# Performance work log

Measured on AMD Instinct MI355X. Metric: run time of the kernel, lower is better.

## Reference

```python
import jax, jax.numpy as jnp
import numpy as np

N_NODES = 50000
N_EDGES = 800000
D_IN = 128
D_OUT = 128
NEG_SLOPE = 0.2


def setup_inputs() -> dict:
    key = jax.random.key(0)
    ks = jax.random.split(key, 6)
    stdv = 1.0 / np.sqrt(D_OUT)
    X = jax.random.normal(ks[0], (N_NODES, D_IN), dtype=jnp.float32)
    W = jax.random.uniform(ks[1], (D_IN, D_OUT), dtype=jnp.float32, minval=-stdv, maxval=stdv)
    W_r = jax.random.uniform(ks[2], (D_IN, D_OUT), dtype=jnp.float32, minval=-stdv, maxval=stdv)
    W_l = jax.random.uniform(ks[3], (D_IN, D_OUT), dtype=jnp.float32, minval=-stdv, maxval=stdv)
    src = jax.random.randint(ks[4], (N_EDGES,), 0, N_NODES, dtype=jnp.int32)
    dst = jax.random.randint(ks[5], (N_EDGES,), 0, N_NODES, dtype=jnp.int32)
    return {"X": X, "W": W, "W_r": W_r, "W_l": W_l, "src": src, "dst": dst}


def reference(X, W, W_r, W_l, src, dst):
    # Dense transforms (comb/agg feature paths)
    comb = X @ W            # [N, D_out]
    h_r = X @ W_r           # [N, D_out]
    h_l = X @ W_l           # [N, D_out]
    # SDDMM: per-edge score e_ij = dot(h_l[i], h_r[j]) at nonzeros of A
    e = jnp.sum(h_l[src] * h_r[dst], axis=-1)          # [E]
    e = jax.nn.leaky_relu(e, negative_slope=NEG_SLOPE)  # LeakyReLU(0.2) on edge values
    # SpMM aggregation: agg[i] = sum_{j in N(i)} e_ij * comb[j]
    msgs = e[:, None] * comb[dst]                       # [E, D_out]
    agg = jax.ops.segment_sum(msgs, src, num_segments=N_NODES)  # [N, D_out]
    return agg
```

## Files before the change

kernel.cpp:

```cpp
#include <hip/hip_runtime.h>
#include <hip/hip_bf16.h>

#define N_NODES 50000
#define N_EDGES 800000
#define D 128
#define NEG_SLOPE 0.2f
#define APAD 136

#define FB 196
#define BCAP 8192
#define CHUNK 4096
#define BIN_NBLK ((N_EDGES + CHUNK - 1) / CHUNK)
#define GROWS 64
#define GGRID ((N_NODES + GROWS - 1) / GROWS)

typedef __attribute__((ext_vector_type(8))) short bf16x8;
typedef __attribute__((ext_vector_type(4))) float f32x4;

__device__ inline unsigned short f2bf(float f) {
    union { float f; unsigned u; } v; v.f = f;
    const unsigned r = v.u + 0x7FFF + ((v.u >> 16) & 1);
    return (unsigned short)(r >> 16);
}
__device__ inline unsigned fbits(float f) { union { float f; unsigned u; } v; v.f = f; return v.u; }
__device__ inline float ffrom(unsigned u) { union { unsigned u; float f; } v; v.u = u; return v.f; }

__device__ inline void unpack8(const float4 raw, float* o) {
    const unsigned w0 = fbits(raw.x), w1 = fbits(raw.y), w2 = fbits(raw.z), w3 = fbits(raw.w);
    o[0] = ffrom(w0 << 16); o[1] = ffrom(w0 & 0xffff0000u);
    o[2] = ffrom(w1 << 16); o[3] = ffrom(w1 & 0xffff0000u);
    o[4] = ffrom(w2 << 16); o[5] = ffrom(w2 & 0xffff0000u);
    o[6] = ffrom(w3 << 16); o[7] = ffrom(w3 & 0xffff0000u);
}

__device__ inline int scan256_incl(int* arr, int t, int v) {
    arr[t] = v; __syncthreads();
#pragma unroll
    for (int off = 1; off < 256; off <<= 1) {
        const int u = (t >= off) ? arr[t - off] : 0;
        __syncthreads();
        arr[t] += u;
        __syncthreads();
    }
    return arr[t];
}

__device__ __forceinline__ void stage_B_lds(unsigned short* Bs, const ushort* __restrict__ BT) {
    const int tid = threadIdx.x;
#pragma unroll
    for (int i = 0; i < 8; ++i) {
        const int idx = tid + i * 256;
        const int row = idx >> 4;
        const int c8 = (idx & 15) << 3;
        const float4 v = ((const float4*)BT)[idx];
        *(float4*)&Bs[row * APAD + c8] = v;
    }
}

template <bool OUT_F32>
__device__ __forceinline__ void mfma_from_lds(const unsigned short* Bs,
                                              const unsigned short* As,
                                              int rb, float* __restrict__ Cf,
                                              ushort* __restrict__ Cb, int nrows) {
    const int tid = threadIdx.x;
    const int w = tid >> 6, lane = tid & 63, m = lane & 15, kq = lane >> 4;
    f32x4 acc[8] = {};
    const unsigned short* Arow = &As[(w * 16 + m) * APAD + kq * 8];
#pragma unroll
    for (int kc = 0; kc < 4; ++kc) {
        const bf16x8 af = *(const bf16x8*)(Arow + kc * 32);
#pragma unroll
        for (int t2 = 0; t2 < 8; ++t2) {
            const bf16x8 bf = *(const bf16x8*)&Bs[(t2 * 16 + m) * APAD + kc * 32 + kq * 8];
            acc[t2] = __builtin_amdgcn_mfma_f32_16x16x32_bf16(af, bf, acc[t2], 0, 0, 0);
        }
    }
    const int orow0 = rb + w * 16 + kq * 4;
#pragma unroll
    for (int t2 = 0; t2 < 8; ++t2) {
#pragma unroll
        for (int r = 0; r < 4; ++r) {
            const int row = orow0 + r;
            if (row < nrows) {
                const size_t o = (size_t)row * D + t2 * 16 + m;
                if (OUT_F32) Cf[o] = acc[t2][r];
                else         Cb[o] = f2bf(acc[t2][r]);
            }
        }
    }
}

__global__ __launch_bounds__(256) void bin_prep_kernel(const int* __restrict__ src,
                                                       const int* __restrict__ dst,
                                                       int* __restrict__ bucket_fill,
                                                       int2* __restrict__ binned,
                                                       const float* __restrict__ W_l,
                                                       const float* __restrict__ W_r,
                                                       const float* __restrict__ W,
                                                       ushort* __restrict__ MbT,
                                                       ushort* __restrict__ WbT) {
    if (blockIdx.x < BIN_NBLK) {
        __shared__ int hist[256];
        __shared__ int bstart[256];
        __shared__ int reserveS[256];
        __shared__ int fillL[256];
        __shared__ int2 pairs[CHUNK];
        __shared__ int targ[CHUNK];
        const int t = threadIdx.x;
        const int e0 = blockIdx.x * CHUNK;

        hist[t] = 0;
        __syncthreads();

        int s[16], d[16], b[16];
#pragma unroll
        for (int i = 0; i < 16; ++i) {
            const int e = e0 + i * 256 + t;
            if (e < N_EDGES) {
                s[i] = src[e]; d[i] = dst[e]; b[i] = s[i] >> 8;
                atomicAdd(&hist[b[i]], 1);
            } else b[i] = -1;
        }
        __syncthreads();
        const int hv = hist[t];
        const int incl = scan256_incl(bstart, t, hv);
        const int mystart = incl - hv;
        reserveS[t] = hv ? atomicAdd(&bucket_fill[t], hv) : 0;
        __syncthreads();
        bstart[t] = mystart;
        fillL[t] = mystart;
        __syncthreads();
#pragma unroll
        for (int i = 0; i < 16; ++i) {
            if (b[i] >= 0) {
                const int p = atomicAdd(&fillL[b[i]], 1);
                pairs[p] = make_int2(s[i], d[i]);
                const int pos = reserveS[b[i]] + (p - bstart[b[i]]);
                targ[p] = (pos < BCAP) ? (b[i] * BCAP + pos) : -1;
            }
        }
        __syncthreads();
        const int nval = min(CHUNK, N_EDGES - e0);
        for (int j = t; j < nval; j += 256)
            if (targ[j] >= 0) binned[targ[j]] = pairs[j];
    } else {
        const int a = (blockIdx.x - BIN_NBLK) * 2 + (threadIdx.x >> 7);
        const int b2 = threadIdx.x & 127;
        float acc = 0.f;
#pragma unroll
        for (int c = 0; c < D; c += 4) {
            const float4 wl = *(const float4*)(W_l + a * D + c);
            const float4 wr = *(const float4*)(W_r + b2 * D + c);
            acc += wl.x * wr.x + wl.y * wr.y + wl.z * wr.z + wl.w * wr.w;
        }
        MbT[b2 * D + a] = f2bf(acc);
        WbT[b2 * D + a] = f2bf(W[a * D + b2]);
    }
}

__global__ __launch_bounds__(256) void convert_gemm1_kernel(const float4* __restrict__ Xf4,
                                                            ushort* __restrict__ Xb,
                                                            const ushort* __restrict__ MbT,
                                                            ushort* __restrict__ hMb) {
    __shared__ __align__(16) unsigned short Bs[D * APAD];
    __shared__ __align__(16) unsigned short As[GROWS * APAD];
    const int t = threadIdx.x;
    const int rb = blockIdx.x * GROWS;

    stage_B_lds(Bs, MbT);

#pragma unroll
    for (int i = 0; i < 4; ++i) {
        const int f2 = t + i * 256;
        const int row = f2 >> 4;
        const int c8 = (f2 & 15) << 3;
        ushort4 lo = {0, 0, 0, 0}, hi = {0, 0, 0, 0};
        if (rb + row < N_NODES) {
            const float4 a = Xf4[(size_t)(rb + row) * 32 + (c8 >> 2)];
            const float4 b = Xf4[(size_t)(rb + row) * 32 + (c8 >> 2) + 1];
            lo.x = f2bf(a.x); lo.y = f2bf(a.y); lo.z = f2bf(a.z); lo.w = f2bf(a.w);
            hi.x = f2bf(b.x); hi.y = f2bf(b.y); hi.z = f2bf(b.z); hi.w = f2bf(b.w);
            ushort* gp = Xb + (size_t)(rb + row) * D + c8;
            *(ushort4*)gp = lo;
            *(ushort4*)(gp + 4) = hi;
        }
        *(ushort4*)&As[row * APAD + c8] = lo;
        *(ushort4*)&As[row * APAD + c8 + 4] = hi;
    }
    __syncthreads();
    mfma_from_lds<false>(Bs, As, rb, nullptr, hMb, N_NODES);
}

__global__ __launch_bounds__(256) void fine_kernel(const int2* __restrict__ binned,
                                                   const int* __restrict__ bucket_fill,
                                                   int* __restrict__ offsets,
                                                   int* __restrict__ sorted_dst) {
    __shared__ int cntS[256];
    __shared__ int nh[256];
    __shared__ int ex[256];
    __shared__ int fill[256];
    __shared__ int dstbuf[BCAP];
    const int b = blockIdx.x;
    const int t = threadIdx.x;

    const int myc = (t < FB) ? bucket_fill[t] : 0;
    scan256_incl(cntS, t, myc);
    const int base = (b == 0) ? 0 : cntS[b - 1];
    int cnt = cntS[b] - base;
    if (cnt > BCAP) cnt = BCAP;

    nh[t] = 0;
    __syncthreads();
    const int2* bb = binned + (size_t)b * BCAP;
    for (int e = t; e < cnt; e += 256) atomicAdd(&nh[bb[e].x & 255], 1);
    __syncthreads();
    const int v = nh[t];
    const int incl2 = scan256_incl(ex, t, v);
    const int mystart = incl2 - v;
    const int node = b * 256 + t;
    if (node < N_NODES) offsets[node] = base + mystart;
    fill[t] = mystart;
    __syncthreads();
    for (int e = t; e < cnt; e += 256) {
        const int2 sd = bb[e];
        const int p = atomicAdd(&fill[sd.x & 255], 1);
        dstbuf[p] = sd.y;
    }
    __syncthreads();
    for (int j = t; j < cnt; j += 256)
        sorted_dst[base + j] = dstbuf[j];
}

__global__ __launch_bounds__(256) void spmm_gemm2_kernel(const ushort* __restrict__ hMb,
                                                         const ushort* __restrict__ Xb,
                                                         const int* __restrict__ offsets,
                                                         const int* __restrict__ sorted_dst,
                                                         const ushort* __restrict__ WbT,
                                                         float* __restrict__ agg) {
    __shared__ __align__(16) unsigned short Bs[D * APAD];
    __shared__ __align__(16) unsigned short aggl[GROWS * APAD];
    const int t = threadIdx.x;
    const int rb = blockIdx.x * GROWS;
    const int lane = t & 63, w = t >> 6;
    const int q = lane >> 4, ql = lane & 15;
    const int qid = w * 4 + q;

    stage_B_lds(Bs, WbT);

    for (int i = 0; i < 4; ++i) {
        const int node = rb + qid * 4 + i;
        float acc[8] = {0.f, 0.f, 0.f, 0.f, 0.f, 0.f, 0.f, 0.f};
        if (node < N_NODES) {
            float hm[8];
            unpack8(*(const float4*)(hMb + (size_t)node * D + ql * 8), hm);
            const int start = offsets[node];
            const int end = (node == N_NODES - 1) ? N_EDGES : offsets[node + 1];
            int idx = start;
            while (idx + 3 < end) {
                const int d0 = sorted_dst[idx];
                const int d1 = sorted_dst[idx + 1];
                const int d2 = sorted_dst[idx + 2];
                const int d3 = sorted_dst[idx + 3];
                const float4 r0 = *(const float4*)(Xb + (size_t)d0 * D + ql * 8);
                const float4 r1 = *(const float4*)(Xb + (size_t)d1 * D + ql * 8);
                const float4 r2 = *(const float4*)(Xb + (size_t)d2 * D + ql * 8);
                const float4 r3 = *(const float4*)(Xb + (size_t)d3 * D + ql * 8);
                float t0 = 0.f, t1 = 0.f, t2 = 0.f, t3 = 0.f;
                {
                    float x[8];
                    unpack8(r0, x);
#pragma unroll
                    for (int j = 0; j < 8; ++j) t0 = fmaf(hm[j], x[j], t0);
                    unpack8(r1, x);
#pragma unroll
                    for (int j = 0; j < 8; ++j) t1 = fmaf(hm[j], x[j], t1);
                    unpack8(r2, x);
#pragma unroll
                    for (int j = 0; j < 8; ++j) t2 = fmaf(hm[j], x[j], t2);
                    unpack8(r3, x);
#pragma unroll
                    for (int j = 0; j < 8; ++j) t3 = fmaf(hm[j], x[j], t3);
                }
#pragma unroll
                for (int mm = 1; mm < 16; mm <<= 1) {
                    t0 += __shfl_xor(t0, mm);
                    t1 += __shfl_xor(t1, mm);
                    t2 += __shfl_xor(t2, mm);
                    t3 += __shfl_xor(t3, mm);
                }
                const float e0 = t0 > 0.f ? t0 : NEG_SLOPE * t0;
                const float e1 = t1 > 0.f ? t1 : NEG_SLOPE * t1;
                const float e2 = t2 > 0.f ? t2 : NEG_SLOPE * t2;
                const float e3 = t3 > 0.f ? t3 : NEG_SLOPE * t3;
                {
                    float x[8];
                    unpack8(r0, x);
#pragma unroll
                    for (int j = 0; j < 8; ++j) acc[j] = fmaf(e0, x[j], acc[j]);
                    unpack8(r1, x);
#pragma unroll
                    for (int j = 0; j < 8; ++j) acc[j] = fmaf(e1, x[j], acc[j]);
                    unpack8(r2, x);
#pragma unroll
                    for (int j = 0; j < 8; ++j) acc[j] = fmaf(e2, x[j], acc[j]);
                    unpack8(r3, x);
#pragma unroll
                    for (int j = 0; j < 8; ++j) acc[j] = fmaf(e3, x[j], acc[j]);
                }
                idx += 4;
            }
            while (idx < end) {
                const int d0 = sorted_dst[idx];
                const float4 r0 = *(const float4*)(Xb + (size_t)d0 * D + ql * 8);
                float x[8];
                unpack8(r0, x);
                float t0 = 0.f;
#pragma unroll
                for (int j = 0; j < 8; ++j) t0 = fmaf(hm[j], x[j], t0);
#pragma unroll
                for (int mm = 1; mm < 16; mm <<= 1) t0 += __shfl_xor(t0, mm);
                const float e0 = t0 > 0.f ? t0 : NEG_SLOPE * t0;
#pragma unroll
                for (int j = 0; j < 8; ++j) acc[j] = fmaf(e0, x[j], acc[j]);
                ++idx;
            }
        }
        ushort4 o0, o1;
        o0.x = f2bf(acc[0]); o0.y = f2bf(acc[1]); o0.z = f2bf(acc[2]); o0.w = f2bf(acc[3]);
        o1.x = f2bf(acc[4]); o1.y = f2bf(acc[5]); o1.z = f2bf(acc[6]); o1.w = f2bf(acc[7]);
        unsigned short* lp = &aggl[(qid * 4 + i) * APAD + ql * 8];
        *(ushort4*)lp = o0;
        *(ushort4*)(lp + 4) = o1;
    }
    __syncthreads();
    mfma_from_lds<true>(Bs, aggl, rb, agg, nullptr, N_NODES);
}

extern "C" void kernel_launch(void* const* d_in, const int* in_sizes, int n_in,
                              void* d_out, int out_size, void* d_ws, size_t ws_size,
                              hipStream_t stream) {
    const float* X   = (const float*)d_in[0];
    const float* W   = (const float*)d_in[1];
    const float* W_r = (const float*)d_in[2];
    const float* W_l = (const float*)d_in[3];
    const int* src   = (const int*)d_in[4];
    const int* dst   = (const int*)d_in[5];
    float* agg = (float*)d_out;

    ushort* Xb          = (ushort*)d_ws;
    ushort* hMb         = Xb + (size_t)N_NODES * D;
    ushort* MbT         = hMb + (size_t)N_NODES * D;
    ushort* WbT         = MbT + D * D;
    int*    offsets     = (int*)(WbT + D * D);
    int*    sorted_dst  = offsets + N_NODES;
    int*    bucket_fill = sorted_dst + N_EDGES;
    int2*   binned      = (int2*)(bucket_fill + 256);

    hipMemsetAsync(bucket_fill, 0, 256 * sizeof(int), stream);

    bin_prep_kernel<<<BIN_NBLK + 64, 256, 0, stream>>>(
        src, dst, bucket_fill, binned, W_l, W_r, W, MbT, WbT);

    fine_kernel<<<FB, 256, 0, stream>>>(binned, bucket_fill, offsets, sorted_dst);

    convert_gemm1_kernel<<<GGRID, 256, 0, stream>>>(
        (const float4*)X, Xb, MbT, hMb);

    spmm_gemm2_kernel<<<GGRID, 256, 0, stream>>>(
        hMb, Xb, offsets, sorted_dst, WbT, agg);
}
```

Measured before the change: 185.7 us.

## Restructure pipeline: fuse binning with GEMM1, split SpMM per-wave from GEMM2

Weight precomputation moves into a small prep kernel that also zeroes bucket counters, which removes the memset. Edge binning now runs in the same launch as the X conversion and first GEMM, using a shared LDS union and smaller chunks. The SpMM becomes one wave per node with four edge lanes, reduced by shuffles, and writes bf16 aggregates to a buffer that a separate GEMM2 kernel consumes. The fine sort uses 512 threads. This trades an extra global round trip of the aggregates and one more launch for better load balance and parallelism in the gather.

Measured after the change: 169.6 us. 8.7% less time.

```diff
diff --git a/kernel.cpp b/kernel.cpp
--- a/kernel.cpp
+++ b/kernel.cpp
@@ -9,10 +9,11 @@
 
 #define FB 196
 #define BCAP 8192
-#define CHUNK 4096
+#define CHUNK 2048
 #define BIN_NBLK ((N_EDGES + CHUNK - 1) / CHUNK)
 #define GROWS 64
 #define GGRID ((N_NODES + GROWS - 1) / GROWS)
+#define GEMM_LDS (D * APAD * 2 + GROWS * APAD * 2)
 
 typedef __attribute__((ext_vector_type(8))) short bf16x8;
 typedef __attribute__((ext_vector_type(4))) float f32x4;
@@ -90,31 +91,53 @@
     }
 }
 
-__global__ __launch_bounds__(256) void bin_prep_kernel(const int* __restrict__ src,
-                                                       const int* __restrict__ dst,
-                                                       int* __restrict__ bucket_fill,
-                                                       int2* __restrict__ binned,
-                                                       const float* __restrict__ W_l,
-                                                       const float* __restrict__ W_r,
-                                                       const float* __restrict__ W,
-                                                       ushort* __restrict__ MbT,
-                                                       ushort* __restrict__ WbT) {
-    if (blockIdx.x < BIN_NBLK) {
-        __shared__ int hist[256];
-        __shared__ int bstart[256];
-        __shared__ int reserveS[256];
-        __shared__ int fillL[256];
-        __shared__ int2 pairs[CHUNK];
-        __shared__ int targ[CHUNK];
-        const int t = threadIdx.x;
-        const int e0 = blockIdx.x * CHUNK;
+__global__ __launch_bounds__(256) void prep_kernel(const float* __restrict__ W_l,
+                                                   const float* __restrict__ W_r,
+                                                   const float* __restrict__ W,
+                                                   ushort* __restrict__ MbT,
+                                                   ushort* __restrict__ WbT,
+                                                   int* __restrict__ bucket_fill) {
+    if (blockIdx.x == 0) bucket_fill[threadIdx.x] = 0;
+    const int a = blockIdx.x * 2 + (threadIdx.x >> 7);
+    const int b2 = threadIdx.x & 127;
+    float acc = 0.f;
+#pragma unroll
+    for (int c = 0; c < D; c += 4) {
+        const float4 wl = *(const float4*)(W_l + a * D + c);
+        const float4 wr = *(const float4*)(W_r + b2 * D + c);
+        acc += wl.x * wr.x + wl.y * wr.y + wl.z * wr.z + wl.w * wr.w;
+    }
+    MbT[b2 * D + a] = f2bf(acc);
+    WbT[b2 * D + a] = f2bf(W[a * D + b2]);
+}
+
+__global__ __launch_bounds__(256) void k1_kernel(const int* __restrict__ src,
+                                                 const int* __restrict__ dst,
+                                                 int* __restrict__ bucket_fill,
+                                                 int2* __restrict__ binned,
+                                                 const ushort* __restrict__ MbT,
+                                                 const float4* __restrict__ Xf4,
+                                                 ushort* __restrict__ Xb,
+                                                 ushort* __restrict__ hMb) {
+    __shared__ __align__(16) char smem[GEMM_LDS];
+    const int bx = blockIdx.x;
+    const int t = threadIdx.x;
+
+    if (bx < BIN_NBLK) {
+        int*  hist     = (int*)smem;
+        int*  bstart   = hist + 256;
+        int*  reserveS = bstart + 256;
+        int*  fillL    = reserveS + 256;
+        int2* pairs    = (int2*)(fillL + 256);
+        int*  targ     = (int*)(pairs + CHUNK);
+        const int e0 = bx * CHUNK;
 
         hist[t] = 0;
         __syncthreads();
 
-        int s[16], d[16], b[16];
-#pragma unroll
-        for (int i = 0; i < 16; ++i) {
+        int s[8], d[8], b[8];
+#pragma unroll
+        for (int i = 0; i < 8; ++i) {
             const int e = e0 + i * 256 + t;
             if (e < N_EDGES) {
                 s[i] = src[e]; d[i] = dst[e]; b[i] = s[i] >> 8;
@@ -131,7 +154,7 @@
         fillL[t] = mystart;
         __syncthreads();
 #pragma unroll
-        for (int i = 0; i < 16; ++i) {
+        for (int i = 0; i < 8; ++i) {
             if (b[i] >= 0) {
                 const int p = atomicAdd(&fillL[b[i]], 1);
                 pairs[p] = make_int2(s[i], d[i]);
@@ -144,54 +167,35 @@
         for (int j = t; j < nval; j += 256)
             if (targ[j] >= 0) binned[targ[j]] = pairs[j];
     } else {
-        const int a = (blockIdx.x - BIN_NBLK) * 2 + (threadIdx.x >> 7);
-        const int b2 = threadIdx.x & 127;
-        float acc = 0.f;
-#pragma unroll
-        for (int c = 0; c < D; c += 4) {
-            const float4 wl = *(const float4*)(W_l + a * D + c);
-            const float4 wr = *(const float4*)(W_r + b2 * D + c);
-            acc += wl.x * wr.x + wl.y * wr.y + wl.z * wr.z + wl.w * wr.w;
-        }
-        MbT[b2 * D + a] = f2bf(acc);
-        WbT[b2 * D + a] = f2bf(W[a * D + b2]);
-    }
-}
-
-__global__ __launch_bounds__(256) void convert_gemm1_kernel(const float4* __restrict__ Xf4,
-                                                            ushort* __restrict__ Xb,
-                                                            const ushort* __restrict__ MbT,
-                                                            ushort* __restrict__ hMb) {
-    __shared__ __align__(16) unsigned short Bs[D * APAD];
-    __shared__ __align__(16) unsigned short As[GROWS * APAD];
-    const int t = threadIdx.x;
-    const int rb = blockIdx.x * GROWS;
-
-    stage_B_lds(Bs, MbT);
-
-#pragma unroll
-    for (int i = 0; i < 4; ++i) {
-        const int f2 = t + i * 256;
-        const int row = f2 >> 4;
-        const int c8 = (f2 & 15) << 3;
-        ushort4 lo = {0, 0, 0, 0}, hi = {0, 0, 0, 0};
-        if (rb + row < N_NODES) {
-            const float4 a = Xf4[(size_t)(rb + row) * 32 + (c8 >> 2)];
-            const float4 b = Xf4[(size_t)(rb + row) * 32 + (c8 >> 2) + 1];
-            lo.x = f2bf(a.x); lo.y = f2bf(a.y); lo.z = f2bf(a.z); lo.w = f2bf(a.w);
-            hi.x = f2bf(b.x); hi.y = f2bf(b.y); hi.z = f2bf(b.z); hi.w = f2bf(b.w);
-            ushort* gp = Xb + (size_t)(rb + row) * D + c8;
-            *(ushort4*)gp = lo;
-            *(ushort4*)(gp + 4) = hi;
-        }
-        *(ushort4*)&As[row * APAD + c8] = lo;
-        *(ushort4*)&As[row * APAD + c8 + 4] = hi;
-    }
-    __syncthreads();
-    mfma_from_lds<false>(Bs, As, rb, nullptr, hMb, N_NODES);
-}
-
-__global__ __launch_bounds__(256) void fine_kernel(const int2* __restrict__ binned,
+        unsigned short* Bs = (unsigned short*)smem;
+        unsigned short* As = Bs + D * APAD;
+        const int rb = (bx - BIN_NBLK) * GROWS;
+
+        stage_B_lds(Bs, MbT);
+#pragma unroll
+        for (int i = 0; i < 4; ++i) {
+            const int f2 = t + i * 256;
+            const int row = f2 >> 4;
+            const int c8 = (f2 & 15) << 3;
+            ushort4 lo = {0, 0, 0, 0}, hi = {0, 0, 0, 0};
+            if (rb + row < N_NODES) {
+                const float4 a = Xf4[(size_t)(rb + row) * 32 + (c8 >> 2)];
+                const float4 b = Xf4[(size_t)(rb + row) * 32 + (c8 >> 2) + 1];
+                lo.x = f2bf(a.x); lo.y = f2bf(a.y); lo.z = f2bf(a.z); lo.w = f2bf(a.w);
+                hi.x = f2bf(b.x); hi.y = f2bf(b.y); hi.z = f2bf(b.z); hi.w = f2bf(b.w);
+                ushort* gp = Xb + (size_t)(rb + row) * D + c8;
+                *(ushort4*)gp = lo;
+                *(ushort4*)(gp + 4) = hi;
+            }
+            *(ushort4*)&As[row * APAD + c8] = lo;
+            *(ushort4*)&As[row * APAD + c8 + 4] = hi;
+        }
+        __syncthreads();
+        mfma_from_lds<false>(Bs, As, rb, nullptr, hMb, N_NODES);
+    }
+}
+
+__global__ __launch_bounds__(512) void fine_kernel(const int2* __restrict__ binned,
                                                    const int* __restrict__ bucket_fill,
                                                    int* __restrict__ offsets,
                                                    int* __restrict__ sorted_dst) {
@@ -203,137 +207,177 @@
     const int b = blockIdx.x;
     const int t = threadIdx.x;
 
-    const int myc = (t < FB) ? bucket_fill[t] : 0;
-    scan256_incl(cntS, t, myc);
+    if (t < 256) cntS[t] = (t < FB) ? bucket_fill[t] : 0;
+    __syncthreads();
+#pragma unroll
+    for (int off = 1; off < 256; off <<= 1) {
+        const int u = (t >= off && t < 256) ? cntS[t - off] : 0;
+        __syncthreads();
+        if (t < 256) cntS[t] += u;
+        __syncthreads();
+    }
     const int base = (b == 0) ? 0 : cntS[b - 1];
     int cnt = cntS[b] - base;
     if (cnt > BCAP) cnt = BCAP;
 
-    nh[t] = 0;
+    if (t < 256) nh[t] = 0;
     __syncthreads();
     const int2* bb = binned + (size_t)b * BCAP;
-    for (int e = t; e < cnt; e += 256) atomicAdd(&nh[bb[e].x & 255], 1);
-    __syncthreads();
-    const int v = nh[t];
-    const int incl2 = scan256_incl(ex, t, v);
-    const int mystart = incl2 - v;
-    const int node = b * 256 + t;
-    if (node < N_NODES) offsets[node] = base + mystart;
-    fill[t] = mystart;
-    __syncthreads();
-    for (int e = t; e < cnt; e += 256) {
+    for (int e = t; e < cnt; e += 512) atomicAdd(&nh[bb[e].x & 255], 1);
+    __syncthreads();
+    const int v = (t < 256) ? nh[t] : 0;
+    if (t < 256) ex[t] = v;
+    __syncthreads();
+#pragma unroll
+    for (int off = 1; off < 256; off <<= 1) {
+        const int u = (t >= off && t < 256) ? ex[t - off] : 0;
+        __syncthreads();
+        if (t < 256) ex[t] += u;
+        __syncthreads();
+    }
+    if (t < 256) {
+        const int mystart = ex[t] - v;
+        const int node = b * 256 + t;
+        if (node < N_NODES) offsets[node] = base + mystart;
+        fill[t] = mystart;
+    }
+    __syncthreads();
+    for (int e = t; e < cnt; e += 512) {
         const int2 sd = bb[e];
         const int p = atomicAdd(&fill[sd.x & 255], 1);
         dstbuf[p] = sd.y;
     }
     __syncthreads();
-    for (int j = t; j < cnt; j += 256)
+    for (int j = t; j < cnt; j += 512)
         sorted_dst[base + j] = dstbuf[j];
 }
 
-__global__ __launch_bounds__(256) void spmm_gemm2_kernel(const ushort* __restrict__ hMb,
-                                                         const ushort* __restrict__ Xb,
-                                                         const int* __restrict__ offsets,
-                                                         const int* __restrict__ sorted_dst,
-                                                         const ushort* __restrict__ WbT,
-                                                         float* __restrict__ agg) {
-    __shared__ __align__(16) unsigned short Bs[D * APAD];
-    __shared__ __align__(16) unsigned short aggl[GROWS * APAD];
-    const int t = threadIdx.x;
-    const int rb = blockIdx.x * GROWS;
-    const int lane = t & 63, w = t >> 6;
-    const int q = lane >> 4, ql = lane & 15;
-    const int qid = w * 4 + q;
-
-    stage_B_lds(Bs, WbT);
-
-    for (int i = 0; i < 4; ++i) {
-        const int node = rb + qid * 4 + i;
-        float acc[8] = {0.f, 0.f, 0.f, 0.f, 0.f, 0.f, 0.f, 0.f};
-        if (node < N_NODES) {
-            float hm[8];
-            unpack8(*(const float4*)(hMb + (size_t)node * D + ql * 8), hm);
-            const int start = offsets[node];
-            const int end = (node == N_NODES - 1) ? N_EDGES : offsets[node + 1];
-            int idx = start;
-            while (idx + 3 < end) {
-                const int d0 = sorted_dst[idx];
-                const int d1 = sorted_dst[idx + 1];
-                const int d2 = sorted_dst[idx + 2];
-                const int d3 = sorted_dst[idx + 3];
-                const float4 r0 = *(const float4*)(Xb + (size_t)d0 * D + ql * 8);
-                const float4 r1 = *(const float4*)(Xb + (size_t)d1 * D + ql * 8);
-                const float4 r2 = *(const float4*)(Xb + (size_t)d2 * D + ql * 8);
-                const float4 r3 = *(const float4*)(Xb + (size_t)d3 * D + ql * 8);
-                float t0 = 0.f, t1 = 0.f, t2 = 0.f, t3 = 0.f;
-                {
-                    float x[8];
-                    unpack8(r0, x);
-#pragma unroll
-                    for (int j = 0; j < 8; ++j) t0 = fmaf(hm[j], x[j], t0);
-                    unpack8(r1, x);
-#pragma unroll
-                    for (int j = 0; j < 8; ++j) t1 = fmaf(hm[j], x[j], t1);
-                    unpack8(r2, x);
-#pragma unroll
-                    for (int j = 0; j < 8; ++j) t2 = fmaf(hm[j], x[j], t2);
-                    unpack8(r3, x);
-#pragma unroll
-                    for (int j = 0; j < 8; ++j) t3 = fmaf(hm[j], x[j], t3);
-                }
-#pragma unroll
-                for (int mm = 1; mm < 16; mm <<= 1) {
-                    t0 += __shfl_xor(t0, mm);
-                    t1 += __shfl_xor(t1, mm);
-                    t2 += __shfl_xor(t2, mm);
-                    t3 += __shfl_xor(t3, mm);
-                }
-                const float e0 = t0 > 0.f ? t0 : NEG_SLOPE * t0;
-                const float e1 = t1 > 0.f ? t1 : NEG_SLOPE * t1;
-                const float e2 = t2 > 0.f ? t2 : NEG_SLOPE * t2;
-                const float e3 = t3 > 0.f ? t3 : NEG_SLOPE * t3;
-                {
-                    float x[8];
-                    unpack8(r0, x);
-#pragma unroll
-                    for (int j = 0; j < 8; ++j) acc[j] = fmaf(e0, x[j], acc[j]);
-                    unpack8(r1, x);
-#pragma unroll
-                    for (int j = 0; j < 8; ++j) acc[j] = fmaf(e1, x[j], acc[j]);
-                    unpack8(r2, x);
-#pragma unroll
-                    for (int j = 0; j < 8; ++j) acc[j] = fmaf(e2, x[j], acc[j]);
-                    unpack8(r3, x);
-#pragma unroll
-                    for (int j = 0; j < 8; ++j) acc[j] = fmaf(e3, x[j], acc[j]);
-                }
-                idx += 4;
-            }
-            while (idx < end) {
-                const int d0 = sorted_dst[idx];
-                const float4 r0 = *(const float4*)(Xb + (size_t)d0 * D + ql * 8);
-                float x[8];
-                unpack8(r0, x);
-                float t0 = 0.f;
-#pragma unroll
-                for (int j = 0; j < 8; ++j) t0 = fmaf(hm[j], x[j], t0);
-#pragma unroll
-                for (int mm = 1; mm < 16; mm <<= 1) t0 += __shfl_xor(t0, mm);
-                const float e0 = t0 > 0.f ? t0 : NEG_SLOPE * t0;
-#pragma unroll
-                for (int j = 0; j < 8; ++j) acc[j] = fmaf(e0, x[j], acc[j]);
-                ++idx;
-            }
-        }
+__global__ __launch_bounds__(256) void spmm_kernel(const ushort* __restrict__ hMb,
+                                                   const ushort* __restrict__ Xb,
+                                                   const int* __restrict__ offsets,
+                                                   const int* __restrict__ sorted_dst,
+                                                   ushort* __restrict__ aggXb) {
+    const int wave = threadIdx.x >> 6;
+    const int lane = threadIdx.x & 63;
+    const int node = blockIdx.x * 4 + wave;
+    const int q = lane >> 4;
+    const int ql = lane & 15;
+
+    float hm[8];
+    unpack8(*(const float4*)(hMb + (size_t)node * D + ql * 8), hm);
+
+    const int start = offsets[node];
+    const int end = (node == N_NODES - 1) ? N_EDGES : offsets[node + 1];
+
+    float acc[8] = {0.f, 0.f, 0.f, 0.f, 0.f, 0.f, 0.f, 0.f};
+
+    int idx = start + q;
+    while (idx + 12 < end) {
+        const int d0 = sorted_dst[idx];
+        const int d1 = sorted_dst[idx + 4];
+        const int d2 = sorted_dst[idx + 8];
+        const int d3 = sorted_dst[idx + 12];
+        const float4 r0 = *(const float4*)(Xb + (size_t)d0 * D + ql * 8);
+        const float4 r1 = *(const float4*)(Xb + (size_t)d1 * D + ql * 8);
+        const float4 r2 = *(const float4*)(Xb + (size_t)d2 * D + ql * 8);
+        const float4 r3 = *(const float4*)(Xb + (size_t)d3 * D + ql * 8);
+        float t0 = 0.f, t1 = 0.f, t2 = 0.f, t3 = 0.f;
+        {
+            float x[8];
+            unpack8(r0, x);
+#pragma unroll
+            for (int j = 0; j < 8; ++j) t0 = fmaf(hm[j], x[j], t0);
+            unpack8(r1, x);
+#pragma unroll
+            for (int j = 0; j < 8; ++j) t1 = fmaf(hm[j], x[j], t1);
+            unpack8(r2, x);
+#pragma unroll
+            for (int j = 0; j < 8; ++j) t2 = fmaf(hm[j], x[j], t2);
+            unpack8(r3, x);
+#pragma unroll
+            for (int j = 0; j < 8; ++j) t3 = fmaf(hm[j], x[j], t3);
+        }
+#pragma unroll
+        for (int mm = 1; mm < 16; mm <<= 1) {
+            t0 += __shfl_xor(t0, mm);
+            t1 += __shfl_xor(t1, mm);
+            t2 += __shfl_xor(t2, mm);
+            t3 += __shfl_xor(t3, mm);
+        }
+        const float e0 = t0 > 0.f ? t0 : NEG_SLOPE * t0;
+        const float e1 = t1 > 0.f ? t1 : NEG_SLOPE * t1;
+        const float e2 = t2 > 0.f ? t2 : NEG_SLOPE * t2;
+        const float e3 = t3 > 0.f ? t3 : NEG_SLOPE * t3;
+        {
+            float x[8];
+            unpack8(r0, x);
+#pragma unroll
+            for (int j = 0; j < 8; ++j) acc[j] = fmaf(e0, x[j], acc[j]);
+            unpack8(r1, x);
+#pragma unroll
+            for (int j = 0; j < 8; ++j) acc[j] = fmaf(e1, x[j], acc[j]);
+            unpack8(r2, x);
+#pragma unroll
+            for (int j = 0; j < 8; ++j) acc[j] = fmaf(e2, x[j], acc[j]);
+            unpack8(r3, x);
+#pragma unroll
+            for (int j = 0; j < 8; ++j) acc[j] = fmaf(e3, x[j], acc[j]);
+        }
+        idx += 16;
+    }
+    while (idx < end) {
+        const int d0 = sorted_dst[idx];
+        const float4 r0 = *(const float4*)(Xb + (size_t)d0 * D + ql * 8);
+        float x[8];
+        unpack8(r0, x);
+        float t0 = 0.f;
+#pragma unroll
+        for (int j = 0; j < 8; ++j) t0 = fmaf(hm[j], x[j], t0);
+#pragma unroll
+        for (int mm = 1; mm < 16; mm <<= 1) t0 += __shfl_xor(t0, mm);
+        const float e0 = t0 > 0.f ? t0 : NEG_SLOPE * t0;
+#pragma unroll
+        for (int j = 0; j < 8; ++j) acc[j] = fmaf(e0, x[j], acc[j]);
+        idx += 4;
+    }
+
+#pragma unroll
+    for (int j = 0; j < 8; ++j) {
+        acc[j] += __shfl_xor(acc[j], 16);
+        acc[j] += __shfl_xor(acc[j], 32);
+    }
+    if (q == 0) {
         ushort4 o0, o1;
         o0.x = f2bf(acc[0]); o0.y = f2bf(acc[1]); o0.z = f2bf(acc[2]); o0.w = f2bf(acc[3]);
         o1.x = f2bf(acc[4]); o1.y = f2bf(acc[5]); o1.z = f2bf(acc[6]); o1.w = f2bf(acc[7]);
-        unsigned short* lp = &aggl[(qid * 4 + i) * APAD + ql * 8];
-        *(ushort4*)lp = o0;
-        *(ushort4*)(lp + 4) = o1;
-    }
-    __syncthreads();
-    mfma_from_lds<true>(Bs, aggl, rb, agg, nullptr, N_NODES);
+        ushort* outp = aggXb + (size_t)node * D + ql * 8;
+        *(ushort4*)outp = o0;
+        *(ushort4*)(outp + 4) = o1;
+    }
+}
+
+__global__ __launch_bounds__(256) void gemm2_kernel(const ushort* __restrict__ A,
+                                                    const ushort* __restrict__ BT,
+                                                    float* __restrict__ Cf) {
+    __shared__ __align__(16) char smem[GEMM_LDS];
+    unsigned short* Bs = (unsigned short*)smem;
+    unsigned short* As = Bs + D * APAD;
+    const int tid = threadIdx.x;
+    const int rb = blockIdx.x * GROWS;
+
+    stage_B_lds(Bs, BT);
+#pragma unroll
+    for (int i = 0; i < 4; ++i) {
+        const int idx = tid + i * 256;
+        const int row = idx >> 4;
+        const int c8 = (idx & 15) << 3;
+        float4 v = {0.f, 0.f, 0.f, 0.f};
+        if (rb + row < N_NODES)
+            v = ((const float4*)(A + (size_t)(rb + row) * D))[idx & 15];
+        *(float4*)&As[row * APAD + c8] = v;
+    }
+    __syncthreads();
+    mfma_from_lds<true>(Bs, As, rb, Cf, nullptr, N_NODES);
 }
 
 extern "C" void kernel_launch(void* const* d_in, const int* in_sizes, int n_in,
@@ -349,23 +393,22 @@
 
     ushort* Xb          = (ushort*)d_ws;
     ushort* hMb         = Xb + (size_t)N_NODES * D;
-    ushort* MbT         = hMb + (size_t)N_NODES * D;
+    ushort* aggXb       = hMb + (size_t)N_NODES * D;
+    ushort* MbT         = aggXb + (size_t)N_NODES * D;
     ushort* WbT         = MbT + D * D;
     int*    offsets     = (int*)(WbT + D * D);
     int*    sorted_dst  = offsets + N_NODES;
     int*    bucket_fill = sorted_dst + N_EDGES;
     int2*   binned      = (int2*)(bucket_fill + 256);
 
-    hipMemsetAsync(bucket_fill, 0, 256 * sizeof(int), stream);
-
-    bin_prep_kernel<<<BIN_NBLK + 64, 256, 0, stream>>>(
-        src, dst, bucket_fill, binned, W_l, W_r, W, MbT, WbT);
-
-    fine_kernel<<<FB, 256, 0, stream>>>(binned, bucket_fill, offsets, sorted_dst);
-
-    convert_gemm1_kernel<<<GGRID, 256, 0, stream>>>(
-        (const float4*)X, Xb, MbT, hMb);
-
-    spmm_gemm2_kernel<<<GGRID, 256, 0, stream>>>(
-        hMb, Xb, offsets, sorted_dst, WbT, agg);
-}
+    prep_kernel<<<64, 256, 0, stream>>>(W_l, W_r, W, MbT, WbT, bucket_fill);
+
+    k1_kernel<<<BIN_NBLK + GGRID, 256, 0, stream>>>(
+        src, dst, bucket_fill, binned, MbT, (const float4*)X, Xb, hMb);
+
+    fine_kernel<<<FB, 512, 0, stream>>>(binned, bucket_fill, offsets, sorted_dst);
+
+    spmm_kernel<<<N_NODES / 4, 256, 0, stream>>>(hMb, Xb, offsets, sorted_dst, aggXb);
+
+    gemm2_kernel<<<GGRID, 256, 0, stream>>>(aggXb, WbT, agg);
+}
```
